# Kernel optimization log

Hardware: AMD Instinct MI355X
Metric: run time of the kernel (lower is better)

Reference implementation:

```python
import jax, jax.numpy as jnp
import numpy as np

BETA = 0.85
THRESHOLD = 1.0
T, B = 1000, 256
N_IN, N_HID, N_OUT = 3, 200, 1


def setup_inputs() -> dict:
    key = jax.random.key(0)
    k0, k1, k2, k3 = jax.random.split(key, 4)
    inputs = jax.random.normal(k0, (T, B, N_IN), dtype=jnp.float32)
    # Learned parameters (nn.Linear weights are [out, in]; snntorch RLeaky
    # all_to_all recurrent is a Linear(N_HID, N_HID) with bias).
    W1 = jax.random.normal(k1, (N_HID, N_IN), dtype=jnp.float32) * 0.3
    b1 = jnp.zeros((N_HID,), jnp.float32)
    Wrec = jax.random.normal(k2, (N_HID, N_HID), dtype=jnp.float32) * 0.05
    brec = jnp.zeros((N_HID,), jnp.float32)
    W2 = jax.random.normal(k3, (N_OUT, N_HID), dtype=jnp.float32) * 0.1
    b2 = jnp.zeros((N_OUT,), jnp.float32)
    return dict(inputs=inputs, W1=W1, b1=b1, Wrec=Wrec, brec=brec, W2=W2, b2=b2)


def reference(inputs, W1, b1, Wrec, brec, W2, b2):
    # RLeaky (snntorch) with zero reset:
    #   reset   = heaviside(mem_prev - threshold)          (from old mem)
    #   base    = beta*mem_prev + cur1 + Wrec@spk_prev + brec
    #   mem_new = base - reset * base
    #   spk_new = heaviside(mem_new - threshold)
    batch = inputs.shape[1]
    nhid = W1.shape[0]

    def step(carry, x_t):
        spk, mem = carry
        cur1 = x_t @ W1.T + b1                      # [B, N_HID]
        base = BETA * mem + cur1 + spk @ Wrec.T + brec
        reset = (mem > THRESHOLD).astype(mem.dtype)
        mem_new = base - reset * base               # zero reset
        spk_new = (mem_new > THRESHOLD).astype(mem.dtype)
        cur2 = spk_new @ W2.T + b2                  # [B, N_OUT]
        return (spk_new, mem_new), (cur2, spk_new)

    init = (jnp.zeros((batch, nhid), inputs.dtype),
            jnp.zeros((batch, nhid), inputs.dtype))
    _, (cur2_rec, spk1_rec) = jax.lax.scan(step, init, inputs)
    return cur2_rec, spk1_rec  # [T,B,1], [T,B,200]
```

## Files before the change

### kernel.cpp

```cpp
#include <hip/hip_runtime.h>

#define T_STEPS 1000
#define BATCH   256
#define NHID    200
#define ROWF    200
#define BETA_C  0.85f
#define THR_C   1.0f


__launch_bounds__(256, 1)
__global__ void rsnn_kernel(const float* __restrict__ X,
                            const float* __restrict__ W1,
                            const float* __restrict__ b1,
                            const float* __restrict__ Wrec,
                            const float* __restrict__ brec,
                            float* __restrict__ out_spk) {
#pragma clang fp contract(off)
    __shared__ float WT2[NHID * ROWF];
    __shared__ float part[4][4][50];

    const int tid = threadIdx.x;
    const int l   = tid & 63;
    const int w   = tid >> 6;
    const int b   = blockIdx.x;

    for (int idx = tid; idx < NHID * NHID; idx += 256) {
        int r  = idx / NHID;
        int i  = idx - r * NHID;
        int lo = r % 50, k = r / 50;
        WT2[i * ROWF + lo * 4 + k] = Wrec[idx];
    }
    __syncthreads();

    const int lc = (l < 50) ? l : 49;
    const int oc = 50 * w + lc;
    const float w10 = W1[oc * 3 + 0], w11 = W1[oc * 3 + 1], w12 = W1[oc * 3 + 2];
    const float b1j = b1[oc], brj = brec[oc];

    float mem = 0.f;
    unsigned long long bm = 0;

    const float* xp = X + (size_t)b * 3;
    float x0 = xp[0], x1 = xp[1], x2 = xp[2];

    const float* ldsrow  = WT2 + (size_t)lc * 4;
    const int    wbase   = 50 * w;
    float*       spk_out = out_spk + (size_t)b * NHID + wbase + lc;

#define REC_WORD(MASK, BASE)                                                          \
    {                                                                                 \
        unsigned long long m = (MASK);                                                \
        while (m) {                                                                   \
            int i0 = __builtin_ctzll(m); m &= m - 1;                                  \
            bool h1 = m != 0; int i1 = h1 ? __builtin_ctzll(m) : i0; if (h1) m &= m - 1; \
            bool h2 = m != 0; int i2 = h2 ? __builtin_ctzll(m) : i0; if (h2) m &= m - 1; \
            bool h3 = m != 0; int i3 = h3 ? __builtin_ctzll(m) : i0; if (h3) m &= m - 1; \
            const float4 v0 = *(const float4*)(ldsrow + (i0 + (BASE)) * ROWF);        \
            const float4 v1 = *(const float4*)(ldsrow + (i1 + (BASE)) * ROWF);        \
            const float4 v2 = *(const float4*)(ldsrow + (i2 + (BASE)) * ROWF);        \
            const float4 v3 = *(const float4*)(ldsrow + (i3 + (BASE)) * ROWF);        \
            pr0 += v0.x; pr1 += v0.y; pr2 += v0.z; pr3 += v0.w;                       \
            if (h1) { pr0 += v1.x; pr1 += v1.y; pr2 += v1.z; pr3 += v1.w; }           \
            if (h2) { pr0 += v2.x; pr1 += v2.y; pr2 += v2.z; pr3 += v2.w; }           \
            if (h3) { pr0 += v3.x; pr1 += v3.y; pr2 += v3.z; pr3 += v3.w; }           \
        }                                                                             \
    }

    for (int t = 0; t < T_STEPS; ++t) {
        int   tn  = (t + 1 < T_STEPS) ? t + 1 : t;
        float nx0 = xp[(size_t)tn * BATCH * 3 + 0];
        float nx1 = xp[(size_t)tn * BATCH * 3 + 1];
        float nx2 = xp[(size_t)tn * BATCH * 3 + 2];

        float pr0 = 0.f, pr1 = 0.f, pr2 = 0.f, pr3 = 0.f;
        REC_WORD(bm, wbase)

        if (l < 50) {
            part[0][w][l] = pr0;
            part[1][w][l] = pr1;
            part[2][w][l] = pr2;
            part[3][w][l] = pr3;
        }
        asm volatile("s_waitcnt lgkmcnt(0)\n\ts_barrier" ::: "memory");

        float rec = ((part[w][0][lc] + part[w][1][lc])
                     + part[w][2][lc]) + part[w][3][lc];
        asm volatile("s_waitcnt lgkmcnt(0)\n\ts_barrier" ::: "memory");

        float c1 = fmaf(x2, w12, fmaf(x1, w11, x0 * w10)) + b1j;
        float ba = ((BETA_C * mem + c1) + rec) + brj;
        float nm = (mem > THR_C) ? 0.f : ba;
        float sp = (nm > THR_C) ? 1.f : 0.f;
        mem = nm;

        if (l < 50)
            spk_out[(size_t)t * BATCH * NHID] = sp;
        bm = __ballot((l < 50) && (sp > 0.5f));

        x0 = nx0; x1 = nx1; x2 = nx2;
    }
#undef REC_WORD
}

__launch_bounds__(256)
__global__ void cur2_kernel(const float* __restrict__ spk,
                            const float* __restrict__ W2,
                            const float* __restrict__ b2,
                            float* __restrict__ out) {
    const int lane = threadIdx.x & 63;
    const int wid  = (int)((blockIdx.x * blockDim.x + threadIdx.x) >> 6);
    const int nw   = (int)((gridDim.x * blockDim.x) >> 6);

    float4 w2v = {0.f, 0.f, 0.f, 0.f};
    if (lane < 50) w2v = *(const float4*)(W2 + lane * 4);
    const float b2v = b2[0];

    for (int p = wid; p < T_STEPS * BATCH; p += nw) {
        float4 sv = {0.f, 0.f, 0.f, 0.f};
        if (lane < 50) sv = *(const float4*)(spk + (size_t)p * NHID + lane * 4);
        float a = fmaf(sv.w, w2v.w, fmaf(sv.z, w2v.z,
                  fmaf(sv.y, w2v.y, sv.x * w2v.x)));
#pragma unroll
        for (int o = 32; o >= 1; o >>= 1) a += __shfl_xor(a, o);
        if (lane == 0) out[p] = a + b2v;
    }
}

extern "C" void kernel_launch(void* const* d_in, const int* in_sizes, int n_in,
                              void* d_out, int out_size, void* d_ws, size_t ws_size,
                              hipStream_t stream) {
    const float* X    = (const float*)d_in[0];
    const float* W1   = (const float*)d_in[1];
    const float* b1   = (const float*)d_in[2];
    const float* Wrec = (const float*)d_in[3];
    const float* brec = (const float*)d_in[4];
    const float* W2   = (const float*)d_in[5];
    const float* b2   = (const float*)d_in[6];

    float* out_cur2 = (float*)d_out;
    float* out_spk  = (float*)d_out + (size_t)T_STEPS * BATCH;

    rsnn_kernel<<<BATCH, 256, 0, stream>>>(X, W1, b1, Wrec, brec, out_spk);
    cur2_kernel<<<1024, 256, 0, stream>>>(out_spk, W2, b2, out_cur2);
}
```

Measured before the change: 601.9 us.

## Remove second per-step barrier via alternating transposed partial-sum buffer layout

Unrolls the time loop by two and alternates between two index orderings of the shared partial-sum array, so each warp only overwrites cells that it read itself in the previous step. This removes the write-after-read barrier, leaving one workgroup barrier per time step instead of two. The cost is a larger unrolled body and a subtle cross-step ownership invariant that must hold for correctness.

After: 563.5 us. -6.4%, faster.

```diff
diff --git a/kernel.cpp b/kernel.cpp
--- a/kernel.cpp
+++ b/kernel.cpp
@@ -7,6 +7,9 @@
 #define BETA_C  0.85f
 #define THR_C   1.0f
 
+
+#define BARRIER_LGKM \
+    asm volatile("s_waitcnt lgkmcnt(0)\n\ts_barrier" ::: "memory");
 
 __launch_bounds__(256, 1)
 __global__ void rsnn_kernel(const float* __restrict__ X,
@@ -66,39 +69,45 @@
         }                                                                             \
     }
 
-    for (int t = 0; t < T_STEPS; ++t) {
-        int   tn  = (t + 1 < T_STEPS) ? t + 1 : t;
-        float nx0 = xp[(size_t)tn * BATCH * 3 + 0];
-        float nx1 = xp[(size_t)tn * BATCH * 3 + 1];
-        float nx2 = xp[(size_t)tn * BATCH * 3 + 2];
+#define STEP(T, WR0, WR1, WR2, WR3, RD0, RD1, RD2, RD3)                  \
+    {                                                                    \
+        const int t = (T);                                               \
+        int   tn  = (t + 1 < T_STEPS) ? t + 1 : t;                       \
+        float nx0 = xp[(size_t)tn * BATCH * 3 + 0];                      \
+        float nx1 = xp[(size_t)tn * BATCH * 3 + 1];                      \
+        float nx2 = xp[(size_t)tn * BATCH * 3 + 2];                      \
+                                                                         \
+        float pr0 = 0.f, pr1 = 0.f, pr2 = 0.f, pr3 = 0.f;                \
+        REC_WORD(bm, wbase)                                              \
+                                                                         \
+        if (l < 50) { WR0 = pr0; WR1 = pr1; WR2 = pr2; WR3 = pr3; }      \
+        BARRIER_LGKM                                                     \
+                                                                         \
+        float p0 = RD0, p1 = RD1, p2 = RD2, p3 = RD3;                    \
+        float rec = ((p0 + p1) + p2) + p3;                               \
+                                                                         \
+        float c1 = fmaf(x2, w12, fmaf(x1, w11, x0 * w10)) + b1j;         \
+        float ba = ((BETA_C * mem + c1) + rec) + brj;                    \
+        float nm = (mem > THR_C) ? 0.f : ba;                             \
+        float sp = (nm > THR_C) ? 1.f : 0.f;                             \
+        mem = nm;                                                        \
+                                                                         \
+        if (l < 50)                                                      \
+            spk_out[(size_t)t * BATCH * NHID] = sp;                      \
+        bm = __ballot((l < 50) && (sp > 0.5f));                          \
+                                                                         \
+        x0 = nx0; x1 = nx1; x2 = nx2;                                    \
+    }
 
-        float pr0 = 0.f, pr1 = 0.f, pr2 = 0.f, pr3 = 0.f;
-        REC_WORD(bm, wbase)
-
-        if (l < 50) {
-            part[0][w][l] = pr0;
-            part[1][w][l] = pr1;
-            part[2][w][l] = pr2;
-            part[3][w][l] = pr3;
-        }
-        asm volatile("s_waitcnt lgkmcnt(0)\n\ts_barrier" ::: "memory");
-
-        float rec = ((part[w][0][lc] + part[w][1][lc])
-                     + part[w][2][lc]) + part[w][3][lc];
-        asm volatile("s_waitcnt lgkmcnt(0)\n\ts_barrier" ::: "memory");
-
-        float c1 = fmaf(x2, w12, fmaf(x1, w11, x0 * w10)) + b1j;
-        float ba = ((BETA_C * mem + c1) + rec) + brj;
-        float nm = (mem > THR_C) ? 0.f : ba;
-        float sp = (nm > THR_C) ? 1.f : 0.f;
-        mem = nm;
-
-        if (l < 50)
-            spk_out[(size_t)t * BATCH * NHID] = sp;
-        bm = __ballot((l < 50) && (sp > 0.5f));
-
-        x0 = nx0; x1 = nx1; x2 = nx2;
+    for (int tt = 0; tt < T_STEPS; tt += 2) {
+        STEP(tt,
+             part[0][w][l], part[1][w][l], part[2][w][l], part[3][w][l],
+             part[w][0][lc], part[w][1][lc], part[w][2][lc], part[w][3][lc])
+        STEP(tt + 1,
+             part[w][0][l], part[w][1][l], part[w][2][l], part[w][3][l],
+             part[0][w][lc], part[1][w][lc], part[2][w][lc], part[3][w][lc])
     }
+#undef STEP
 #undef REC_WORD
 }
 
```
